# Optimization experiments

Measured on AMD Instinct MI355X. Metric: run time of the kernel, lower is better.

## Reference

```python
import jax, jax.numpy as jnp
import numpy as np

N, E, D, ED = 10000, 320000, 128, 64
EH, EO, NH, NO = 256, 128, 256, 128
EPS = 1e-5


def _ln(x, g, b):
    m = jnp.mean(x, -1, keepdims=True)
    v = jnp.var(x, -1, keepdims=True)
    return (x - m) / jnp.sqrt(v + EPS) * g + b


def _gelu(x):
    return jax.nn.gelu(x, approximate=False)  # torch nn.GELU default is exact erf


def setup_inputs() -> dict:
    key = jax.random.key(0)
    ks = jax.random.split(key, 8)

    def w(k, i, o):
        return jax.random.normal(k, (i, o), jnp.float32) / np.float32(np.sqrt(i))

    return {
        'node_features': jax.random.normal(ks[0], (N, D), jnp.float32),
        'edge_features': jax.random.normal(ks[1], (E, ED), jnp.float32),
        'edge_index': jax.random.randint(ks[2], (2, E), 0, N, jnp.int64),
        'eW1': w(ks[3], 3 * D + 2 + ED, EH), 'eb1': jnp.zeros((EH,), jnp.float32),
        'eg1': jnp.ones((EH,), jnp.float32), 'ebt1': jnp.zeros((EH,), jnp.float32),
        'eW2': w(ks[4], EH, EO), 'eb2': jnp.zeros((EO,), jnp.float32),
        'eg2': jnp.ones((EO,), jnp.float32), 'ebt2': jnp.zeros((EO,), jnp.float32),
        'nW1': w(ks[5], D + EO, NH), 'nb1': jnp.zeros((NH,), jnp.float32),
        'ng1': jnp.ones((NH,), jnp.float32), 'nbt1': jnp.zeros((NH,), jnp.float32),
        'nW2': w(ks[6], NH, NO), 'nb2': jnp.zeros((NO,), jnp.float32),
        'ng2': jnp.ones((NO,), jnp.float32), 'nbt2': jnp.zeros((NO,), jnp.float32),
    }


def reference(node_features, edge_features, edge_index,
              eW1, eb1, eg1, ebt1, eW2, eb2, eg2, ebt2,
              nW1, nb1, ng1, nbt1, nW2, nb2, ng2, nbt2):
    row, col = edge_index[0], edge_index[1]
    src = node_features[row]            # [E, D] gather
    tgt = node_features[col]            # [E, D] gather
    diff = src - tgt                    # node2node_diff: diff + squared norm + norm (D+2)
    radial = jnp.sum(diff * diff, -1, keepdims=True)
    dist = jnp.sqrt(radial + 1e-8)
    cat = jnp.concatenate([src, tgt, diff, radial, dist, edge_features], axis=-1)  # [E, 3D+2+ED]
    h = _gelu(_ln(cat @ eW1 + eb1, eg1, ebt1))
    edge_out = _gelu(_ln(h @ eW2 + eb2, eg2, ebt2))          # [E, EO]
    agg = jax.ops.segment_sum(edge_out, col, num_segments=node_features.shape[0])  # scatter-add
    nh = _gelu(_ln(jnp.concatenate([node_features, agg], -1) @ nW1 + nb1, ng1, nbt1))
    node_out = _gelu(_ln(nh @ nW2 + nb2, ng2, nbt2))          # [N, NO]
    return node_out, edge_out
```

## Files before the change

kernel.cpp:

```cpp
#include <hip/hip_runtime.h>

#define N_NODES 10000
#define N_EDGES 320000
#define DD      128
#define EDF     64
#define EH      256
#define EO      128
#define NH      256
#define NO      128
#define LN_EPS  1e-5f
#define NODE_OUT_SZ (N_NODES * NO)

#define AK    448
#define NKC1  14
#define NKC2  8
#define M_E   64
#define HSTR  264

typedef short s16x8 __attribute__((ext_vector_type(8)));
typedef float f32x4 __attribute__((ext_vector_type(4)));

__device__ __forceinline__ unsigned short f2bf(float f) {
  unsigned int u = __float_as_uint(f);
  u += 0x7FFFu + ((u >> 16) & 1u);
  return (unsigned short)(u >> 16);
}
__device__ __forceinline__ unsigned int pk2(float a, float b) {
  return (unsigned int)f2bf(a) | ((unsigned int)f2bf(b) << 16);
}
__device__ __forceinline__ uint4 pk8(float4 a, float4 b) {
  return make_uint4(pk2(a.x,a.y), pk2(a.z,a.w), pk2(b.x,b.y), pk2(b.z,b.w));
}
__device__ __forceinline__ float gelu_f(float x) {
  float x2 = x * x;
  float p  = __builtin_fmaf(0.044715f * x2, x, x);
  float e  = __expf(-1.5957691216057308f * p);
  return x * __builtin_amdgcn_rcpf(1.0f + e);
}

typedef const __attribute__((address_space(1))) void GV;
typedef __attribute__((address_space(3))) void LV;
__device__ __forceinline__ void gload16(const void* g, void* l) {
  __builtin_amdgcn_global_load_lds((GV*)g, (LV*)l, 16, 0, 0);
}

#define OFF_EW1 0
#define OFF_EW2 114688
#define OFF_NW1 147456
#define OFF_NW2 212992
#define PREP_TOT 245760

__global__ __launch_bounds__(256) void prep_weights(
    const float* __restrict__ eW1, const float* __restrict__ eW2,
    const float* __restrict__ nW1, const float* __restrict__ nW2,
    unsigned short* __restrict__ ws)
{
  int i = blockIdx.x * 256 + threadIdx.x;
  if (i < OFF_EW2) {
    int kc = i >> 13, rem = i & 8191;
    int kq = rem >> 11, rem2 = rem & 2047;
    int col = rem2 >> 3, j = rem2 & 7;
    int k = kc * 32 + kq * 8 + j;
    int kw = (k < 384) ? k : k + 2;
    ws[i] = f2bf(eW1[kw * EH + col]);
  } else if (i < OFF_NW1) {
    int j0 = i - OFF_EW2;
    int kc = j0 >> 12, rem = j0 & 4095;
    int kq = rem >> 10, col = (rem >> 3) & 127, j = rem & 7;
    int k = kc * 32 + kq * 8 + j;
    ws[i] = f2bf(eW2[k * EO + col]);
  } else if (i < OFF_NW2) {
    int j0 = i - OFF_NW1; int c = j0 >> 8, k = j0 & 255;
    ws[i] = f2bf(nW1[k * NH + c]);
  } else if (i < PREP_TOT) {
    int j0 = i - OFF_NW2; int c = j0 >> 8, k = j0 & 255;
    ws[i] = f2bf(nW2[k * NO + c]);
  }
}

__global__ __launch_bounds__(512, 4) void edge_kernel(
    const float* __restrict__ nf, const float* __restrict__ ef,
    const int* __restrict__ ei,
    const float* __restrict__ eW1, const float* __restrict__ eb1,
    const float* __restrict__ eg1, const float* __restrict__ ebt1,
    const float* __restrict__ eb2, const float* __restrict__ eg2,
    const float* __restrict__ ebt2,
    const unsigned short* __restrict__ W1e,
    const unsigned short* __restrict__ W2e,
    float* __restrict__ out)
{
  __shared__ __align__(16) unsigned short Ab[M_E * AK];
  __shared__ __align__(16) unsigned short Bb[8192];
  __shared__ float radL[M_E], distL[M_E];
  __shared__ int   tgtL[M_E];
  __shared__ float sumL[2][M_E], sqL[2][M_E];

  const int tid  = threadIdx.x;
  const int lane = tid & 63;
  const int wave = tid >> 6;
  const int e0   = blockIdx.x * M_E;

  {
    const char* g = (const char*)W1e + wave * 2048 + lane * 16;
    char* l = (char*)Bb + wave * 2048;
    gload16(g, l);
    gload16(g + 1024, l + 1024);
  }

  {
    const int r = tid >> 3, g = tid & 7;
    const int e = e0 + r;
    const int si = ei[e];
    const int ti = ei[N_EDGES + e];
    const float4* sp = (const float4*)(nf + (size_t)si * DD) + g * 4;
    const float4* tp = (const float4*)(nf + (size_t)ti * DD) + g * 4;
    float4 s0 = sp[0], s1 = sp[1], s2 = sp[2], s3 = sp[3];
    float4 t0 = tp[0], t1 = tp[1], t2 = tp[2], t3 = tp[3];
    float4 d0, d1, d2, d3;
    d0.x=s0.x-t0.x; d0.y=s0.y-t0.y; d0.z=s0.z-t0.z; d0.w=s0.w-t0.w;
    d1.x=s1.x-t1.x; d1.y=s1.y-t1.y; d1.z=s1.z-t1.z; d1.w=s1.w-t1.w;
    d2.x=s2.x-t2.x; d2.y=s2.y-t2.y; d2.z=s2.z-t2.z; d2.w=s2.w-t2.w;
    d3.x=s3.x-t3.x; d3.y=s3.y-t3.y; d3.z=s3.z-t3.z; d3.w=s3.w-t3.w;
    float rad = d0.x*d0.x + d0.y*d0.y + d0.z*d0.z + d0.w*d0.w
              + d1.x*d1.x + d1.y*d1.y + d1.z*d1.z + d1.w*d1.w
              + d2.x*d2.x + d2.y*d2.y + d2.z*d2.z + d2.w*d2.w
              + d3.x*d3.x + d3.y*d3.y + d3.z*d3.z + d3.w*d3.w;
    const int rx = r & 7;
    char* Arow = (char*)Ab + r * (AK * 2);
    #define STA(u, v) *(uint4*)(Arow + (((u) & ~7) | (((u) & 7) ^ rx)) * 16) = (v)
    STA(2*g,      pk8(s0, s1));  STA(2*g + 1,  pk8(s2, s3));
    STA(16 + 2*g, pk8(t0, t1));  STA(17 + 2*g, pk8(t2, t3));
    STA(32 + 2*g, pk8(d0, d1));  STA(33 + 2*g, pk8(d2, d3));
    const float4* ep = (const float4*)(ef + (size_t)e * EDF) + g * 2;
    float4 u0 = ep[0], u1 = ep[1];
    STA(48 + g,   pk8(u0, u1));
    #undef STA
    rad += __shfl_xor(rad, 1);
    rad += __shfl_xor(rad, 2);
    rad += __shfl_xor(rad, 4);
    if (g == 0) {
      radL[r]  = rad;
      distL[r] = sqrtf(rad + 1e-8f);
      tgtL[r]  = ti;
    }
  }

  const int wr = wave >> 1, wc = wave & 1;
  const int r4 = lane >> 4, cl = lane & 15;
  const int arow = wr * 16 + cl;
  const int rx = arow & 7;
  const char* Abase = (const char*)Ab + arow * (AK * 2);

  f32x4 acc[8];
#pragma unroll
  for (int t = 0; t < 8; ++t) { f32x4 z = {0.f,0.f,0.f,0.f}; acc[t] = z; }

  __syncthreads();

  for (int kc = 0; ; ) {
    int u = kc * 4 + r4;
    int pu = (u & ~7) | ((u & 7) ^ rx);
    s16x8 af = *(const s16x8*)(Abase + pu * 16);
#pragma unroll
    for (int t = 0; t < 8; ++t) {
      s16x8 bf = *(const s16x8*)((const char*)Bb + r4 * 4096 + (wc * 128 + t * 16 + cl) * 16);
      acc[t] = __builtin_amdgcn_mfma_f32_16x16x32_bf16(af, bf, acc[t], 0, 0, 0);
    }
    if (++kc == NKC1) break;
    __syncthreads();
    {
      const char* g = (const char*)W1e + kc * 16384 + wave * 2048 + lane * 16;
      char* l = (char*)Bb + wave * 2048;
      gload16(g, l);
      gload16(g + 1024, l + 1024);
    }
    __syncthreads();
  }

  float eb1c[8], eg1c[8], ebt1c[8], w4c[8], w5c[8];
#pragma unroll
  for (int t = 0; t < 8; ++t) {
    int c = wc * 128 + t * 16 + cl;
    eb1c[t] = eb1[c]; eg1c[t] = eg1[c]; ebt1c[t] = ebt1[c];
    w4c[t] = eW1[384 * EH + c]; w5c[t] = eW1[385 * EH + c];
  }
  float xs[8][4], mean1[4], inv1[4];
#pragma unroll
  for (int rr = 0; rr < 4; ++rr) {
    int row = wr * 16 + r4 * 4 + rr;
    float rad = radL[row], dst = distL[row];
    float ps = 0.f, pq = 0.f;
#pragma unroll
    for (int t = 0; t < 8; ++t) {
      float x = acc[t][rr] + eb1c[t] + rad * w4c[t] + dst * w5c[t];
      xs[t][rr] = x; ps += x; pq += x * x;
    }
    ps += __shfl_xor(ps, 1); pq += __shfl_xor(pq, 1);
    ps += __shfl_xor(ps, 2); pq += __shfl_xor(pq, 2);
    ps += __shfl_xor(ps, 4); pq += __shfl_xor(pq, 4);
    ps += __shfl_xor(ps, 8); pq += __shfl_xor(pq, 8);
    if (cl == 0) { sumL[wc][row] = ps; sqL[wc][row] = pq; }
  }
  __syncthreads();

  {
    const char* g = (const char*)W2e + wave * 1024 + lane * 16;
    gload16(g, (char*)Bb + wave * 1024);
  }

  unsigned short* hb = (unsigned short*)Ab;
#pragma unroll
  for (int rr = 0; rr < 4; ++rr) {
    int row = wr * 16 + r4 * 4 + rr;
    float s = sumL[0][row] + sumL[1][row];
    float q = sqL[0][row] + sqL[1][row];
    float m = s * (1.f / 256.f);
    float v = q * (1.f / 256.f) - m * m;
    mean1[rr] = m; inv1[rr] = rsqrtf(v + LN_EPS);
  }
#pragma unroll
  for (int t = 0; t < 8; ++t) {
#pragma unroll
    for (int rr = 0; rr < 4; ++rr) {
      int row = wr * 16 + r4 * 4 + rr;
      int c = wc * 128 + t * 16 + cl;
      float y = (xs[t][rr] - mean1[rr]) * inv1[rr] * eg1c[t] + ebt1c[t];
      hb[row * HSTR + c] = f2bf(gelu_f(y));
    }
  }
  __syncthreads();

  f32x4 a2[4];
#pragma unroll
  for (int t = 0; t < 4; ++t) { f32x4 z = {0.f,0.f,0.f,0.f}; a2[t] = z; }

  for (int kc = 0; ; ) {
    s16x8 af = *(const s16x8*)((const char*)hb + arow * (HSTR * 2) + kc * 64 + r4 * 16);
#pragma unroll
    for (int t = 0; t < 4; ++t) {
      s16x8 bf = *(const s16x8*)((const char*)Bb + r4 * 2048 + (wc * 64 + t * 16 + cl) * 16);
      a2[t] = __builtin_amdgcn_mfma_f32_16x16x32_bf16(af, bf, a2[t], 0, 0, 0);
    }
    if (++kc == NKC2) break;
    __syncthreads();
    {
      const char* g = (const char*)W2e + kc * 8192 + wave * 1024 + lane * 16;
      gload16(g, (char*)Bb + wave * 1024);
    }
    __syncthreads();
  }

  float eb2c[4], eg2c[4], ebt2c[4];
#pragma unroll
  for (int t = 0; t < 4; ++t) {
    int c = wc * 64 + t * 16 + cl;
    eb2c[t] = eb2[c]; eg2c[t] = eg2[c]; ebt2c[t] = ebt2[c];
  }
  float xs2[4][4], mean2[4], inv2[4];
#pragma unroll
  for (int rr = 0; rr < 4; ++rr) {
    int row = wr * 16 + r4 * 4 + rr;
    float ps = 0.f, pq = 0.f;
#pragma unroll
    for (int t = 0; t < 4; ++t) {
      float x = a2[t][rr] + eb2c[t];
      xs2[t][rr] = x; ps += x; pq += x * x;
    }
    ps += __shfl_xor(ps, 1); pq += __shfl_xor(pq, 1);
    ps += __shfl_xor(ps, 2); pq += __shfl_xor(pq, 2);
    ps += __shfl_xor(ps, 4); pq += __shfl_xor(pq, 4);
    ps += __shfl_xor(ps, 8); pq += __shfl_xor(pq, 8);
    if (cl == 0) { sumL[wc][row] = ps; sqL[wc][row] = pq; }
  }
  __syncthreads();
#pragma unroll
  for (int rr = 0; rr < 4; ++rr) {
    int row = wr * 16 + r4 * 4 + rr;
    float s = sumL[0][row] + sumL[1][row];
    float q = sqL[0][row] + sqL[1][row];
    float m = s * (1.f / 128.f);
    float v = q * (1.f / 128.f) - m * m;
    mean2[rr] = m; inv2[rr] = rsqrtf(v + LN_EPS);
  }
#pragma unroll
  for (int t = 0; t < 4; ++t) {
#pragma unroll
    for (int rr = 0; rr < 4; ++rr) {
      int row = wr * 16 + r4 * 4 + rr;
      int c = wc * 64 + t * 16 + cl;
      float y = (xs2[t][rr] - mean2[rr]) * inv2[rr] * eg2c[t] + ebt2c[t];
      float val = gelu_f(y);
      int e = e0 + row;
      __builtin_nontemporal_store(val, out + NODE_OUT_SZ + (size_t)e * EO + c);
      atomicAdd(out + (size_t)tgtL[row] * NO + c, val);
    }
  }
}

__global__ __launch_bounds__(256) void node_kernel(
    const float* __restrict__ nf,
    const float* __restrict__ nb1, const float* __restrict__ ng1, const float* __restrict__ nbt1,
    const float* __restrict__ nb2, const float* __restrict__ ng2, const float* __restrict__ nbt2,
    const unsigned short* __restrict__ W1t,
    const unsigned short* __restrict__ W2t,
    float* __restrict__ out)
{
  __shared__ __align__(16) unsigned short Ab[32][HSTR];
  __shared__ __align__(16) unsigned short Bb[256][40];
  __shared__ float sumL[2][32], sqL[2][32];

  const int tid = threadIdx.x;
  const int n0  = blockIdx.x * 32;

  {
    const int r = tid >> 3, g = tid & 7;
    const int node = n0 + r;
    if (node < N_NODES) {
      const float4* xp = (const float4*)(nf  + (size_t)node * DD);
      const float4* ap = (const float4*)(out + (size_t)node * NO);
#pragma unroll
      for (int q = 0; q < 4; ++q) {
        float4 x = xp[g*4 + q]; float4 a = ap[g*4 + q];
        int k0 = g*16 + q*4;
        Ab[r][k0+0]=f2bf(x.x); Ab[r][k0+1]=f2bf(x.y); Ab[r][k0+2]=f2bf(x.z); Ab[r][k0+3]=f2bf(x.w);
        Ab[r][128+k0+0]=f2bf(a.x); Ab[r][128+k0+1]=f2bf(a.y);
        Ab[r][128+k0+2]=f2bf(a.z); Ab[r][128+k0+3]=f2bf(a.w);
      }
    } else {
#pragma unroll
      for (int q = 0; q < 4; ++q) {
        int k0 = g*16 + q*4;
#pragma unroll
        for (int j = 0; j < 4; ++j) { Ab[r][k0+j] = 0; Ab[r][128+k0+j] = 0; }
      }
    }
  }

  const int lane = tid & 63, wave = tid >> 6;
  const int wr = wave >> 1, wc = wave & 1;
  const int r4 = lane >> 4, cl = lane & 15;

  f32x4 acc[8];
#pragma unroll
  for (int t = 0; t < 8; ++t) { f32x4 z = {0.f,0.f,0.f,0.f}; acc[t] = z; }

  __syncthreads();

  for (int kc = 0; kc < 8; ++kc) {
    {
      const uint4* s = (const uint4*)(W1t + (size_t)tid * 256 + kc * 32);
      uint4* d = (uint4*)(&Bb[tid][0]);
      d[0] = s[0]; d[1] = s[1]; d[2] = s[2]; d[3] = s[3];
    }
    __syncthreads();
    s16x8 af = *(const s16x8*)(&Ab[wr*16 + cl][kc*32 + r4*8]);
#pragma unroll
    for (int t = 0; t < 8; ++t) {
      s16x8 bf = *(const s16x8*)(&Bb[wc*128 + t*16 + cl][r4*8]);
      acc[t] = __builtin_amdgcn_mfma_f32_16x16x32_bf16(af, bf, acc[t], 0, 0, 0);
    }
    __syncthreads();
  }

  float b1c[8], g1c[8], bt1c[8];
#pragma unroll
  for (int t = 0; t < 8; ++t) {
    int c = wc*128 + t*16 + cl;
    b1c[t] = nb1[c]; g1c[t] = ng1[c]; bt1c[t] = nbt1[c];
  }
  float xs[8][4], mean1[4], inv1[4];
#pragma unroll
  for (int rr = 0; rr < 4; ++rr) {
    int row = wr*16 + r4*4 + rr;
    float ps = 0.f, pq = 0.f;
#pragma unroll
    for (int t = 0; t < 8; ++t) {
      float x = acc[t][rr] + b1c[t];
      xs[t][rr] = x; ps += x; pq += x * x;
    }
    ps += __shfl_xor(ps, 1); pq += __shfl_xor(pq, 1);
    ps += __shfl_xor(ps, 2); pq += __shfl_xor(pq, 2);
    ps += __shfl_xor(ps, 4); pq += __shfl_xor(pq, 4);
    ps += __shfl_xor(ps, 8); pq += __shfl_xor(pq, 8);
    if (cl == 0) { sumL[wc][row] = ps; sqL[wc][row] = pq; }
  }
  __syncthreads();
  unsigned short* hb = &Ab[0][0];
#pragma unroll
  for (int rr = 0; rr < 4; ++rr) {
    int row = wr*16 + r4*4 + rr;
    float s = sumL[0][row] + sumL[1][row];
    float q = sqL[0][row] + sqL[1][row];
    float m = s * (1.f/256.f);
    float v = q * (1.f/256.f) - m * m;
    mean1[rr] = m; inv1[rr] = rsqrtf(v + LN_EPS);
  }
#pragma unroll
  for (int t = 0; t < 8; ++t) {
#pragma unroll
    for (int rr = 0; rr < 4; ++rr) {
      int row = wr*16 + r4*4 + rr;
      int c = wc*128 + t*16 + cl;
      float y = (xs[t][rr] - mean1[rr]) * inv1[rr] * g1c[t] + bt1c[t];
      hb[row*HSTR + c] = f2bf(gelu_f(y));
    }
  }
  __syncthreads();

  f32x4 a2[4];
#pragma unroll
  for (int t = 0; t < 4; ++t) { f32x4 z = {0.f,0.f,0.f,0.f}; a2[t] = z; }

  for (int kc = 0; kc < 8; ++kc) {
    {
      int c = tid >> 1, hh = tid & 1;
      const uint4* s = (const uint4*)(W2t + (size_t)c * 256 + kc * 32 + hh * 16);
      uint4* d = (uint4*)(&Bb[c][hh * 16]);
      d[0] = s[0]; d[1] = s[1];
    }
    __syncthreads();
    s16x8 af = *(const s16x8*)(hb + (wr*16 + cl) * HSTR + kc*32 + r4*8);
#pragma unroll
    for (int t = 0; t < 4; ++t) {
      s16x8 bf = *(const s16x8*)(&Bb[wc*64 + t*16 + cl][r4*8]);
      a2[t] = __builtin_amdgcn_mfma_f32_16x16x32_bf16(af, bf, a2[t], 0, 0, 0);
    }
    __syncthreads();
  }

  float b2c[4], g2c[4], bt2c[4];
#pragma unroll
  for (int t = 0; t < 4; ++t) {
    int c = wc*64 + t*16 + cl;
    b2c[t] = nb2[c]; g2c[t] = ng2[c]; bt2c[t] = nbt2[c];
  }
  float xs2[4][4], mean2[4], inv2[4];
#pragma unroll
  for (int rr = 0; rr < 4; ++rr) {
    int row = wr*16 + r4*4 + rr;
    float ps = 0.f, pq = 0.f;
#pragma unroll
    for (int t = 0; t < 4; ++t) {
      float x = a2[t][rr] + b2c[t];
      xs2[t][rr] = x; ps += x; pq += x * x;
    }
    ps += __shfl_xor(ps, 1); pq += __shfl_xor(pq, 1);
    ps += __shfl_xor(ps, 2); pq += __shfl_xor(pq, 2);
    ps += __shfl_xor(ps, 4); pq += __shfl_xor(pq, 4);
    ps += __shfl_xor(ps, 8); pq += __shfl_xor(pq, 8);
    if (cl == 0) { sumL[wc][row] = ps; sqL[wc][row] = pq; }
  }
  __syncthreads();
#pragma unroll
  for (int rr = 0; rr < 4; ++rr) {
    int row = wr*16 + r4*4 + rr;
    float s = sumL[0][row] + sumL[1][row];
    float q = sqL[0][row] + sqL[1][row];
    float m = s * (1.f/128.f);
    float v = q * (1.f/128.f) - m * m;
    mean2[rr] = m; inv2[rr] = rsqrtf(v + LN_EPS);
  }
#pragma unroll
  for (int t = 0; t < 4; ++t) {
#pragma unroll
    for (int rr = 0; rr < 4; ++rr) {
      int row = wr*16 + r4*4 + rr;
      int node = n0 + row;
      if (node < N_NODES) {
        int c = wc*64 + t*16 + cl;
        float y = (xs2[t][rr] - mean2[rr]) * inv2[rr] * g2c[t] + bt2c[t];
        out[(size_t)node * NO + c] = gelu_f(y);
      }
    }
  }
}

extern "C" void kernel_launch(void* const* d_in, const int* in_sizes, int n_in,
                              void* d_out, int out_size, void* d_ws, size_t ws_size,
                              hipStream_t stream) {
  const float* nf   = (const float*)d_in[0];
  const float* ef   = (const float*)d_in[1];
  const int*   ei   = (const int*)d_in[2];
  const float* eW1  = (const float*)d_in[3];
  const float* eb1  = (const float*)d_in[4];
  const float* eg1  = (const float*)d_in[5];
  const float* ebt1 = (const float*)d_in[6];
  const float* eW2  = (const float*)d_in[7];
  const float* eb2  = (const float*)d_in[8];
  const float* eg2  = (const float*)d_in[9];
  const float* ebt2 = (const float*)d_in[10];
  const float* nW1  = (const float*)d_in[11];
  const float* nb1  = (const float*)d_in[12];
  const float* ng1  = (const float*)d_in[13];
  const float* nbt1 = (const float*)d_in[14];
  const float* nW2  = (const float*)d_in[15];
  const float* nb2  = (const float*)d_in[16];
  const float* ng2  = (const float*)d_in[17];
  const float* nbt2 = (const float*)d_in[18];
  float* out = (float*)d_out;
  unsigned short* ws = (unsigned short*)d_ws;
  (void)in_sizes; (void)n_in; (void)out_size; (void)ws_size;

  hipMemsetAsync(d_out, 0, (size_t)NODE_OUT_SZ * sizeof(float), stream);

  prep_weights<<<PREP_TOT / 256, 256, 0, stream>>>(eW1, eW2, nW1, nW2, ws);

  edge_kernel<<<N_EDGES / M_E, 512, 0, stream>>>(
      nf, ef, ei, eW1, eb1, eg1, ebt1, eb2, eg2, ebt2,
      ws + OFF_EW1, ws + OFF_EW2, out);

  node_kernel<<<(N_NODES + 31) / 32, 256, 0, stream>>>(
      nf, nb1, ng1, nbt1, nb2, ng2, nbt2,
      ws + OFF_NW1, ws + OFF_NW2, out);
}
```

Before: 523.8 us.

## Fold diff weights into src/tgt weights, double-buffer weight tiles, vectorize stores

The edge input diff=src-tgt is absorbed algebraically into the first-layer weights: the src rows become W_src+W_diff and the tgt rows W_tgt-W_diff. This shrinks K from 448 to 320 and drops the diff columns from shared memory. Both edge and node GEMM loops now double-buffer the weight tiles, with async global-to-LDS loads issued one chunk ahead, halving barriers per chunk. The node kernel is rewritten to use the swizzled LDS layout and direct LDS loads, and output stores are paired into 8-byte writes via lane shuffles. The enlarged LDS buffer may reduce occupancy, and the folded weights are rounded to bf16 after summation, which changes the numerics slightly.

```diff
diff --git a/kernel.cpp b/kernel.cpp
--- a/kernel.cpp
+++ b/kernel.cpp
@@ -11,19 +11,18 @@
 #define LN_EPS  1e-5f
 #define NODE_OUT_SZ (N_NODES * NO)
 
-#define AK    448
-#define NKC1  14
-#define NKC2  8
-#define M_E   64
-#define HSTR  264
+#define AK      320
+#define NKC1    10
+#define NKC2    8
+#define ME_TILE 64
+#define HSTR    264
 
 typedef short s16x8 __attribute__((ext_vector_type(8)));
 typedef float f32x4 __attribute__((ext_vector_type(4)));
+typedef float f32x2 __attribute__((ext_vector_type(2)));
 
 __device__ __forceinline__ unsigned short f2bf(float f) {
-  unsigned int u = __float_as_uint(f);
-  u += 0x7FFFu + ((u >> 16) & 1u);
-  return (unsigned short)(u >> 16);
+  return __builtin_bit_cast(unsigned short, (__bf16)f);
 }
 __device__ __forceinline__ unsigned int pk2(float a, float b) {
   return (unsigned int)f2bf(a) | ((unsigned int)f2bf(b) << 16);
@@ -45,10 +44,10 @@
 }
 
 #define OFF_EW1 0
-#define OFF_EW2 114688
-#define OFF_NW1 147456
-#define OFF_NW2 212992
-#define PREP_TOT 245760
+#define OFF_EW2 81920
+#define OFF_NW1 114688
+#define OFF_NW2 180224
+#define PREP_TOT 212992
 
 __global__ __launch_bounds__(256) void prep_weights(
     const float* __restrict__ eW1, const float* __restrict__ eW2,
@@ -58,23 +57,31 @@
   int i = blockIdx.x * 256 + threadIdx.x;
   if (i < OFF_EW2) {
     int kc = i >> 13, rem = i & 8191;
-    int kq = rem >> 11, rem2 = rem & 2047;
-    int col = rem2 >> 3, j = rem2 & 7;
+    int kq = rem >> 11, col = (rem >> 3) & 255, j = i & 7;
     int k = kc * 32 + kq * 8 + j;
-    int kw = (k < 384) ? k : k + 2;
-    ws[i] = f2bf(eW1[kw * EH + col]);
+    float v;
+    if (k < 128)       v = eW1[k * EH + col] + eW1[(k + 256) * EH + col];
+    else if (k < 256)  v = eW1[k * EH + col] - eW1[(k + 128) * EH + col];
+    else               v = eW1[(k + 130) * EH + col];
+    ws[i] = f2bf(v);
   } else if (i < OFF_NW1) {
     int j0 = i - OFF_EW2;
     int kc = j0 >> 12, rem = j0 & 4095;
-    int kq = rem >> 10, col = (rem >> 3) & 127, j = rem & 7;
+    int kq = rem >> 10, col = (rem >> 3) & 127, j = j0 & 7;
     int k = kc * 32 + kq * 8 + j;
     ws[i] = f2bf(eW2[k * EO + col]);
   } else if (i < OFF_NW2) {
-    int j0 = i - OFF_NW1; int c = j0 >> 8, k = j0 & 255;
-    ws[i] = f2bf(nW1[k * NH + c]);
+    int j0 = i - OFF_NW1;
+    int kc = j0 >> 13, rem = j0 & 8191;
+    int kq = rem >> 11, col = (rem >> 3) & 255, j = j0 & 7;
+    int k = kc * 32 + kq * 8 + j;
+    ws[i] = f2bf(nW1[k * NH + col]);
   } else if (i < PREP_TOT) {
-    int j0 = i - OFF_NW2; int c = j0 >> 8, k = j0 & 255;
-    ws[i] = f2bf(nW2[k * NO + c]);
+    int j0 = i - OFF_NW2;
+    int kc = j0 >> 12, rem = j0 & 4095;
+    int kq = rem >> 10, col = (rem >> 3) & 127, j = j0 & 7;
+    int k = kc * 32 + kq * 8 + j;
+    ws[i] = f2bf(nW2[k * NO + col]);
   }
 }
 
@@ -89,20 +96,20 @@
     const unsigned short* __restrict__ W2e,
     float* __restrict__ out)
 {
-  __shared__ __align__(16) unsigned short Ab[M_E * AK];
-  __shared__ __align__(16) unsigned short Bb[8192];
-  __shared__ float radL[M_E], distL[M_E];
-  __shared__ int   tgtL[M_E];
-  __shared__ float sumL[2][M_E], sqL[2][M_E];
+  __shared__ __align__(16) unsigned short Ab[ME_TILE * AK];
+  __shared__ __align__(16) char Bbc[32768];
+  __shared__ float radL[ME_TILE], distL[ME_TILE];
+  __shared__ int   tgtL[ME_TILE];
+  __shared__ float sumL[2][ME_TILE], sqL[2][ME_TILE];
 
   const int tid  = threadIdx.x;
   const int lane = tid & 63;
   const int wave = tid >> 6;
-  const int e0   = blockIdx.x * M_E;
+  const int e0   = blockIdx.x * ME_TILE;
 
   {
     const char* g = (const char*)W1e + wave * 2048 + lane * 16;
-    char* l = (char*)Bb + wave * 2048;
+    char* l = Bbc + wave * 2048;
     gload16(g, l);
     gload16(g + 1024, l + 1024);
   }
@@ -116,24 +123,22 @@
     const float4* tp = (const float4*)(nf + (size_t)ti * DD) + g * 4;
     float4 s0 = sp[0], s1 = sp[1], s2 = sp[2], s3 = sp[3];
     float4 t0 = tp[0], t1 = tp[1], t2 = tp[2], t3 = tp[3];
-    float4 d0, d1, d2, d3;
-    d0.x=s0.x-t0.x; d0.y=s0.y-t0.y; d0.z=s0.z-t0.z; d0.w=s0.w-t0.w;
-    d1.x=s1.x-t1.x; d1.y=s1.y-t1.y; d1.z=s1.z-t1.z; d1.w=s1.w-t1.w;
-    d2.x=s2.x-t2.x; d2.y=s2.y-t2.y; d2.z=s2.z-t2.z; d2.w=s2.w-t2.w;
-    d3.x=s3.x-t3.x; d3.y=s3.y-t3.y; d3.z=s3.z-t3.z; d3.w=s3.w-t3.w;
-    float rad = d0.x*d0.x + d0.y*d0.y + d0.z*d0.z + d0.w*d0.w
-              + d1.x*d1.x + d1.y*d1.y + d1.z*d1.z + d1.w*d1.w
-              + d2.x*d2.x + d2.y*d2.y + d2.z*d2.z + d2.w*d2.w
-              + d3.x*d3.x + d3.y*d3.y + d3.z*d3.z + d3.w*d3.w;
+    float d0x=s0.x-t0.x, d0y=s0.y-t0.y, d0z=s0.z-t0.z, d0w=s0.w-t0.w;
+    float d1x=s1.x-t1.x, d1y=s1.y-t1.y, d1z=s1.z-t1.z, d1w=s1.w-t1.w;
+    float d2x=s2.x-t2.x, d2y=s2.y-t2.y, d2z=s2.z-t2.z, d2w=s2.w-t2.w;
+    float d3x=s3.x-t3.x, d3y=s3.y-t3.y, d3z=s3.z-t3.z, d3w=s3.w-t3.w;
+    float rad = d0x*d0x + d0y*d0y + d0z*d0z + d0w*d0w
+              + d1x*d1x + d1y*d1y + d1z*d1z + d1w*d1w
+              + d2x*d2x + d2y*d2y + d2z*d2z + d2w*d2w
+              + d3x*d3x + d3y*d3y + d3z*d3z + d3w*d3w;
     const int rx = r & 7;
     char* Arow = (char*)Ab + r * (AK * 2);
     #define STA(u, v) *(uint4*)(Arow + (((u) & ~7) | (((u) & 7) ^ rx)) * 16) = (v)
     STA(2*g,      pk8(s0, s1));  STA(2*g + 1,  pk8(s2, s3));
     STA(16 + 2*g, pk8(t0, t1));  STA(17 + 2*g, pk8(t2, t3));
-    STA(32 + 2*g, pk8(d0, d1));  STA(33 + 2*g, pk8(d2, d3));
     const float4* ep = (const float4*)(ef + (size_t)e * EDF) + g * 2;
     float4 u0 = ep[0], u1 = ep[1];
-    STA(48 + g,   pk8(u0, u1));
+    STA(32 + g,   pk8(u0, u1));
     #undef STA
     rad += __shfl_xor(rad, 1);
     rad += __shfl_xor(rad, 2);
@@ -157,22 +162,22 @@
 
   __syncthreads();
 
-  for (int kc = 0; ; ) {
+#pragma unroll
+  for (int kc = 0; kc < NKC1; ++kc) {
+    if (kc + 1 < NKC1) {
+      const char* g = (const char*)W1e + (size_t)(kc + 1) * 16384 + wave * 2048 + lane * 16;
+      char* l = Bbc + ((kc + 1) & 1) * 16384 + wave * 2048;
+      gload16(g, l);
+      gload16(g + 1024, l + 1024);
+    }
+    const char* Bcur = Bbc + (kc & 1) * 16384;
     int u = kc * 4 + r4;
     int pu = (u & ~7) | ((u & 7) ^ rx);
     s16x8 af = *(const s16x8*)(Abase + pu * 16);
 #pragma unroll
     for (int t = 0; t < 8; ++t) {
-      s16x8 bf = *(const s16x8*)((const char*)Bb + r4 * 4096 + (wc * 128 + t * 16 + cl) * 16);
+      s16x8 bf = *(const s16x8*)(Bcur + r4 * 4096 + (wc * 128 + t * 16 + cl) * 16);
       acc[t] = __builtin_amdgcn_mfma_f32_16x16x32_bf16(af, bf, acc[t], 0, 0, 0);
-    }
-    if (++kc == NKC1) break;
-    __syncthreads();
-    {
-      const char* g = (const char*)W1e + kc * 16384 + wave * 2048 + lane * 16;
-      char* l = (char*)Bb + wave * 2048;
-      gload16(g, l);
-      gload16(g + 1024, l + 1024);
     }
     __syncthreads();
   }
@@ -205,7 +210,7 @@
 
   {
     const char* g = (const char*)W2e + wave * 1024 + lane * 16;
-    gload16(g, (char*)Bb + wave * 1024);
+    gload16(g, Bbc + wave * 1024);
   }
 
   unsigned short* hb = (unsigned short*)Ab;
@@ -234,18 +239,18 @@
 #pragma unroll
   for (int t = 0; t < 4; ++t) { f32x4 z = {0.f,0.f,0.f,0.f}; a2[t] = z; }
 
-  for (int kc = 0; ; ) {
+#pragma unroll
+  for (int kc = 0; kc < NKC2; ++kc) {
+    if (kc + 1 < NKC2) {
+      const char* g = (const char*)W2e + (size_t)(kc + 1) * 8192 + wave * 1024 + lane * 16;
+      gload16(g, Bbc + ((kc + 1) & 1) * 8192 + wave * 1024);
+    }
+    const char* Bcur = Bbc + (kc & 1) * 8192;
     s16x8 af = *(const s16x8*)((const char*)hb + arow * (HSTR * 2) + kc * 64 + r4 * 16);
 #pragma unroll
     for (int t = 0; t < 4; ++t) {
-      s16x8 bf = *(const s16x8*)((const char*)Bb + r4 * 2048 + (wc * 64 + t * 16 + cl) * 16);
+      s16x8 bf = *(const s16x8*)(Bcur + r4 * 2048 + (wc * 64 + t * 16 + cl) * 16);
       a2[t] = __builtin_amdgcn_mfma_f32_16x16x32_bf16(af, bf, a2[t], 0, 0, 0);
-    }
-    if (++kc == NKC2) break;
-    __syncthreads();
-    {
-      const char* g = (const char*)W2e + kc * 8192 + wave * 1024 + lane * 16;
-      gload16(g, (char*)Bb + wave * 1024);
     }
     __syncthreads();
   }
@@ -290,55 +295,61 @@
       int c = wc * 64 + t * 16 + cl;
       float y = (xs2[t][rr] - mean2[rr]) * inv2[rr] * eg2c[t] + ebt2c[t];
       float val = gelu_f(y);
+      float pv  = __shfl_xor(val, 1);
       int e = e0 + row;
-      __builtin_nontemporal_store(val, out + NODE_OUT_SZ + (size_t)e * EO + c);
       atomicAdd(out + (size_t)tgtL[row] * NO + c, val);
-    }
-  }
-}
-
-__global__ __launch_bounds__(256) void node_kernel(
+      if ((lane & 1) == 0) {
+        f32x2 v2; v2[0] = val; v2[1] = pv;
+        __builtin_nontemporal_store(v2, (f32x2*)(out + NODE_OUT_SZ + (size_t)e * EO + c));
+      }
+    }
+  }
+}
+
+__global__ __launch_bounds__(256, 4) void node_kernel(
     const float* __restrict__ nf,
     const float* __restrict__ nb1, const float* __restrict__ ng1, const float* __restrict__ nbt1,
     const float* __restrict__ nb2, const float* __restrict__ ng2, const float* __restrict__ nbt2,
-    const unsigned short* __restrict__ W1t,
-    const unsigned short* __restrict__ W2t,
+    const unsigned short* __restrict__ W1n,
+    const unsigned short* __restrict__ W2n,
     float* __restrict__ out)
 {
-  __shared__ __align__(16) unsigned short Ab[32][HSTR];
-  __shared__ __align__(16) unsigned short Bb[256][40];
+  __shared__ __align__(16) unsigned short Ab[32 * 256];
+  __shared__ __align__(16) char Bbc[32768];
   __shared__ float sumL[2][32], sqL[2][32];
 
-  const int tid = threadIdx.x;
-  const int n0  = blockIdx.x * 32;
+  const int tid  = threadIdx.x;
+  const int lane = tid & 63;
+  const int wave = tid >> 6;
+  const int n0   = blockIdx.x * 32;
+
+  {
+    const char* g = (const char*)W1n + tid * 16;
+    char* l = Bbc + wave * 1024;
+#pragma unroll
+    for (int s = 0; s < 4; ++s) gload16(g + s * 4096, l + s * 4096);
+  }
 
   {
     const int r = tid >> 3, g = tid & 7;
     const int node = n0 + r;
-    if (node < N_NODES) {
-      const float4* xp = (const float4*)(nf  + (size_t)node * DD);
-      const float4* ap = (const float4*)(out + (size_t)node * NO);
-#pragma unroll
-      for (int q = 0; q < 4; ++q) {
-        float4 x = xp[g*4 + q]; float4 a = ap[g*4 + q];
-        int k0 = g*16 + q*4;
-        Ab[r][k0+0]=f2bf(x.x); Ab[r][k0+1]=f2bf(x.y); Ab[r][k0+2]=f2bf(x.z); Ab[r][k0+3]=f2bf(x.w);
-        Ab[r][128+k0+0]=f2bf(a.x); Ab[r][128+k0+1]=f2bf(a.y);
-        Ab[r][128+k0+2]=f2bf(a.z); Ab[r][128+k0+3]=f2bf(a.w);
-      }
-    } else {
-#pragma unroll
-      for (int q = 0; q < 4; ++q) {
-        int k0 = g*16 + q*4;
-#pragma unroll
-        for (int j = 0; j < 4; ++j) { Ab[r][k0+j] = 0; Ab[r][128+k0+j] = 0; }
-      }
-    }
-  }
-
-  const int lane = tid & 63, wave = tid >> 6;
+    const float4* xp = (const float4*)(nf  + (size_t)node * DD) + g * 4;
+    const float4* ap = (const float4*)(out + (size_t)node * NO) + g * 4;
+    float4 x0 = xp[0], x1 = xp[1], x2 = xp[2], x3 = xp[3];
+    float4 a0 = ap[0], a1 = ap[1], a2v = ap[2], a3 = ap[3];
+    const int rx = r & 7;
+    char* Arow = (char*)Ab + r * 512;
+    #define STN(u, v) *(uint4*)(Arow + (((u) & ~7) | (((u) & 7) ^ rx)) * 16) = (v)
+    STN(2*g,      pk8(x0, x1));  STN(2*g + 1,  pk8(x2, x3));
+    STN(16 + 2*g, pk8(a0, a1));  STN(17 + 2*g, pk8(a2v, a3));
+    #undef STN
+  }
+
   const int wr = wave >> 1, wc = wave & 1;
   const int r4 = lane >> 4, cl = lane & 15;
+  const int arow = wr * 16 + cl;
+  const int rx = arow & 7;
+  const char* Abase = (const char*)Ab + arow * 512;
 
   f32x4 acc[8];
 #pragma unroll
@@ -346,32 +357,36 @@
 
   __syncthreads();
 
+#pragma unroll
   for (int kc = 0; kc < 8; ++kc) {
-    {
-      const uint4* s = (const uint4*)(W1t + (size_t)tid * 256 + kc * 32);
-      uint4* d = (uint4*)(&Bb[tid][0]);
-      d[0] = s[0]; d[1] = s[1]; d[2] = s[2]; d[3] = s[3];
+    if (kc + 1 < 8) {
+      const char* g = (const char*)W1n + (size_t)(kc + 1) * 16384 + tid * 16;
+      char* l = Bbc + ((kc + 1) & 1) * 16384 + wave * 1024;
+#pragma unroll
+      for (int s = 0; s < 4; ++s) gload16(g + s * 4096, l + s * 4096);
+    }
+    const char* Bcur = Bbc + (kc & 1) * 16384;
+    int u = kc * 4 + r4;
+    int pu = (u & ~7) | ((u & 7) ^ rx);
+    s16x8 af = *(const s16x8*)(Abase + pu * 16);
+#pragma unroll
+    for (int t = 0; t < 8; ++t) {
+      s16x8 bf = *(const s16x8*)(Bcur + r4 * 4096 + (wc * 128 + t * 16 + cl) * 16);
+      acc[t] = __builtin_amdgcn_mfma_f32_16x16x32_bf16(af, bf, acc[t], 0, 0, 0);
     }
     __syncthreads();
-    s16x8 af = *(const s16x8*)(&Ab[wr*16 + cl][kc*32 + r4*8]);
-#pragma unroll
-    for (int t = 0; t < 8; ++t) {
-      s16x8 bf = *(const s16x8*)(&Bb[wc*128 + t*16 + cl][r4*8]);
-      acc[t] = __builtin_amdgcn_mfma_f32_16x16x32_bf16(af, bf, acc[t], 0, 0, 0);
-    }
-    __syncthreads();
   }
 
   float b1c[8], g1c[8], bt1c[8];
 #pragma unroll
   for (int t = 0; t < 8; ++t) {
-    int c = wc*128 + t*16 + cl;
+    int c = wc * 128 + t * 16 + cl;
     b1c[t] = nb1[c]; g1c[t] = ng1[c]; bt1c[t] = nbt1[c];
   }
   float xs[8][4], mean1[4], inv1[4];
 #pragma unroll
   for (int rr = 0; rr < 4; ++rr) {
-    int row = wr*16 + r4*4 + rr;
+    int row = wr * 16 + r4 * 4 + rr;
     float ps = 0.f, pq = 0.f;
 #pragma unroll
     for (int t = 0; t < 8; ++t) {
@@ -385,24 +400,34 @@
     if (cl == 0) { sumL[wc][row] = ps; sqL[wc][row] = pq; }
   }
   __syncthreads();
-  unsigned short* hb = &Ab[0][0];
-#pragma unroll
-  for (int rr = 0; rr < 4; ++rr) {
-    int row = wr*16 + r4*4 + rr;
+
+  {
+    const char* g = (const char*)W2n + tid * 16;
+    char* l = Bbc + wave * 1024;
+    gload16(g, l);
+    gload16(g + 4096, l + 4096);
+  }
+
+#pragma unroll
+  for (int rr = 0; rr < 4; ++rr) {
+    int row = wr * 16 + r4 * 4 + rr;
     float s = sumL[0][row] + sumL[1][row];
     float q = sqL[0][row] + sqL[1][row];
-    float m = s * (1.f/256.f);
-    float v = q * (1.f/256.f) - m * m;
+    float m = s * (1.f / 256.f);
+    float v = q * (1.f / 256.f) - m * m;
     mean1[rr] = m; inv1[rr] = rsqrtf(v + LN_EPS);
   }
+  char* hB = (char*)Ab;
 #pragma unroll
   for (int t = 0; t < 8; ++t) {
 #pragma unroll
     for (int rr = 0; rr < 4; ++rr) {
-      int row = wr*16 + r4*4 + rr;
-      int c = wc*128 + t*16 + cl;
+      int row = wr * 16 + r4 * 4 + rr;
+      int c = wc * 128 + t * 16 + cl;
       float y = (xs[t][rr] - mean1[rr]) * inv1[rr] * g1c[t] + bt1c[t];
-      hb[row*HSTR + c] = f2bf(gelu_f(y));
+      int un = c >> 3;
+      int pun = (un & ~7) | ((un & 7) ^ (row & 7));
+      *(unsigned short*)(hB + row * 512 + pun * 16 + (c & 7) * 2) = f2bf(gelu_f(y));
     }
   }
   __syncthreads();
@@ -411,33 +436,36 @@
 #pragma unroll
   for (int t = 0; t < 4; ++t) { f32x4 z = {0.f,0.f,0.f,0.f}; a2[t] = z; }
 
+#pragma unroll
   for (int kc = 0; kc < 8; ++kc) {
-    {
-      int c = tid >> 1, hh = tid & 1;
-      const uint4* s = (const uint4*)(W2t + (size_t)c * 256 + kc * 32 + hh * 16);
-      uint4* d = (uint4*)(&Bb[c][hh * 16]);
-      d[0] = s[0]; d[1] = s[1];
+    if (kc + 1 < 8) {
+      const char* g = (const char*)W2n + (size_t)(kc + 1) * 8192 + tid * 16;
+      char* l = Bbc + ((kc + 1) & 1) * 8192 + wave * 1024;
+      gload16(g, l);
+      gload16(g + 4096, l + 4096);
+    }
+    const char* Bcur = Bbc + (kc & 1) * 8192;
+    int u = kc * 4 + r4;
+    int pu = (u & ~7) | ((u & 7) ^ rx);
+    s16x8 af = *(const s16x8*)(Abase + pu * 16);
+#pragma unroll
+    for (int t = 0; t < 4; ++t) {
+      s16x8 bf = *(const s16x8*)(Bcur + r4 * 2048 + (wc * 64 + t * 16 + cl) * 16);
+      a2[t] = __builtin_amdgcn_mfma_f32_16x16x32_bf16(af, bf, a2[t], 0, 0, 0);
     }
     __syncthreads();
-    s16x8 af = *(const s16x8*)(hb + (wr*16 + cl) * HSTR + kc*32 + r4*8);
-#pragma unroll
-    for (int t = 0; t < 4; ++t) {
-      s16x8 bf = *(const s16x8*)(&Bb[wc*64 + t*16 + cl][r4*8]);
-      a2[t] = __builtin_amdgcn_mfma_f32_16x16x32_bf16(af, bf, a2[t], 0, 0, 0);
-    }
-    __syncthreads();
   }
 
   float b2c[4], g2c[4], bt2c[4];
 #pragma unroll
   for (int t = 0; t < 4; ++t) {
-    int c = wc*64 + t*16 + cl;
+    int c = wc * 64 + t * 16 + cl;
     b2c[t] = nb2[c]; g2c[t] = ng2[c]; bt2c[t] = nbt2[c];
   }
   float xs2[4][4], mean2[4], inv2[4];
 #pragma unroll
   for (int rr = 0; rr < 4; ++rr) {
-    int row = wr*16 + r4*4 + rr;
+    int row = wr * 16 + r4 * 4 + rr;
     float ps = 0.f, pq = 0.f;
 #pragma unroll
     for (int t = 0; t < 4; ++t) {
@@ -453,23 +481,26 @@
   __syncthreads();
 #pragma unroll
   for (int rr = 0; rr < 4; ++rr) {
-    int row = wr*16 + r4*4 + rr;
+    int row = wr * 16 + r4 * 4 + rr;
     float s = sumL[0][row] + sumL[1][row];
     float q = sqL[0][row] + sqL[1][row];
-    float m = s * (1.f/128.f);
-    float v = q * (1.f/128.f) - m * m;
+    float m = s * (1.f / 128.f);
+    float v = q * (1.f / 128.f) - m * m;
     mean2[rr] = m; inv2[rr] = rsqrtf(v + LN_EPS);
   }
 #pragma unroll
   for (int t = 0; t < 4; ++t) {
 #pragma unroll
     for (int rr = 0; rr < 4; ++rr) {
-      int row = wr*16 + r4*4 + rr;
+      int row = wr * 16 + r4 * 4 + rr;
       int node = n0 + row;
-      if (node < N_NODES) {
-        int c = wc*64 + t*16 + cl;
-        float y = (xs2[t][rr] - mean2[rr]) * inv2[rr] * g2c[t] + bt2c[t];
-        out[(size_t)node * NO + c] = gelu_f(y);
+      int c = wc * 64 + t * 16 + cl;
+      float y = (xs2[t][rr] - mean2[rr]) * inv2[rr] * g2c[t] + bt2c[t];
+      float val = gelu_f(y);
+      float pv  = __shfl_xor(val, 1);
+      if (((lane & 1) == 0) && node < N_NODES) {
+        f32x2 v2; v2[0] = val; v2[1] = pv;
+        *(f32x2*)(out + (size_t)node * NO + c) = v2;
       }
     }
   }
@@ -501,11 +532,11 @@
   unsigned short* ws = (unsigned short*)d_ws;
   (void)in_sizes; (void)n_in; (void)out_size; (void)ws_size;
 
-  hipMemsetAsync(d_out, 0, (size_t)NODE_OUT_SZ * sizeof(float), stream);
+  (void)hipMemsetAsync(d_out, 0, (size_t)NODE_OUT_SZ * sizeof(float), stream);
 
   prep_weights<<<PREP_TOT / 256, 256, 0, stream>>>(eW1, eW2, nW1, nW2, ws);
 
-  edge_kernel<<<N_EDGES / M_E, 512, 0, stream>>>(
+  edge_kernel<<<N_EDGES / ME_TILE, 512, 0, stream>>>(
       nf, ef, ei, eW1, eb1, eg1, ebt1, eb2, eg2, ebt2,
       ws + OFF_EW1, ws + OFF_EW2, out);
 
```

Result: no change. 515.5 us (-1.6%).
